# Optimization experiments

Hardware: AMD Instinct MI355X
Metric: run time of the kernel (lower is better)

## Reference

```python
import jax, jax.numpy as jnp
import numpy as np

Q = 256    # ques_size (feat_size)
H = 256    # seq_hidden_size
T = 500000 # history length
K = 32     # attn_k


def setup_inputs() -> dict:
    key = jax.random.key(0)
    ks = jax.random.split(key, 10)
    s = 0.05
    return {
        "ques_h": jax.random.normal(ks[0], (Q,), dtype=jnp.float32),
        "score": jax.random.uniform(ks[1], (1,), dtype=jnp.float32),
        "qs": jax.random.normal(ks[2], (T, Q), dtype=jnp.float32),
        "hs": jax.random.normal(ks[3], (T, H), dtype=jnp.float32),
        # GRU params (torch gate order: reset, update, new)
        "W_ih": jax.random.normal(ks[4], (3 * H, 2 * Q), dtype=jnp.float32) * s,
        "W_hh": jax.random.normal(ks[5], (3 * H, H), dtype=jnp.float32) * s,
        "b_ih": jax.random.normal(ks[6], (3 * H,), dtype=jnp.float32) * s,
        "b_hh": jax.random.normal(ks[7], (3 * H,), dtype=jnp.float32) * s,
        # score_net: Linear(Q + H, 1)
        "W_s": jax.random.normal(ks[8], (1, Q + H), dtype=jnp.float32) * s,
        "b_s": jax.random.normal(ks[9], (1,), dtype=jnp.float32) * s,
        "attn_k": K,
    }


def reference(ques_h, score, qs, hs, W_ih, W_hh, b_ih, b_hh, W_s, b_s, attn_k):
    # --- top-k attention over history ---
    alpha = qs @ ques_h                       # [T] similarity matvec
    vals, idx = jax.lax.top_k(alpha, attn_k)  # k = min(T, attn_k); T >> k
    w = jax.nn.softmax(vals)                  # [k]
    attn_h = w @ hs[idx]                      # gather [k,H] then weighted sum -> [H]

    # --- score prediction ---
    pred = W_s @ jnp.concatenate([ques_h, attn_h]) + b_s  # [1]

    # --- score-gated GRU input ---
    ge = (score >= 0.5).astype(ques_h.dtype)              # [1], broadcasts
    x = jnp.concatenate([ques_h * ge, ques_h * (1.0 - ge)])  # [2Q]

    # --- single-step GRU (torch semantics) ---
    h_prev = hs[-1]                            # [H]
    gi = W_ih @ x + b_ih                       # [3H]
    gh = W_hh @ h_prev + b_hh                  # [3H]
    i_r, i_z, i_n = jnp.split(gi, 3)
    h_r, h_z, h_n = jnp.split(gh, 3)
    r = jax.nn.sigmoid(i_r + h_r)
    z = jax.nn.sigmoid(i_z + h_z)
    n = jnp.tanh(i_n + r * h_n)
    h_new = (1.0 - z) * n + z * h_prev         # [H]

    # --- history append (torch.cat bookkeeping in SP.forward) ---
    qs_new = jnp.concatenate([qs, ques_h[None, :]], axis=0)  # [T+1, Q]
    hs_new = jnp.concatenate([hs, h_new[None, :]], axis=0)   # [T+1, H]
    return (pred, qs_new, hs_new)
```

## Files before the change

kernel.cpp:

```cpp
#include <hip/hip_runtime.h>
#include <math.h>

constexpr int kT = 500000;
constexpr int kQ = 256;
constexpr int kH = 256;
constexpr int kK = 32;
constexpr int kNB1 = 256;
constexpr int kCHUNK = (kT + kNB1 - 1) / kNB1;
constexpr int kNC = kNB1 * kK;

__device__ __forceinline__ void store4(float* __restrict__ dst, float4 v) {
  dst[0] = v.x; dst[1] = v.y; dst[2] = v.z; dst[3] = v.w;
}

__global__ __launch_bounds__(256) void k_copy_qs_alpha(
    const float* __restrict__ qs, const float* __restrict__ qh,
    float* __restrict__ out, float* __restrict__ alpha) {
  const int lane = threadIdx.x & 63;
  const int wid  = (int)((blockIdx.x * blockDim.x + threadIdx.x) >> 6);
  const int nw   = (int)((gridDim.x * blockDim.x) >> 6);
  const float4 q4 = ((const float4*)qh)[lane];
  for (int t = wid; t <= kT; t += nw) {
    const float4* src = (t < kT) ? ((const float4*)(qs + (size_t)t * kQ))
                                 : ((const float4*)qh);
    float4 v = src[lane];
    store4(out + 1 + (size_t)t * kQ + lane * 4, v);
    if (t < kT) {
      float d = v.x * q4.x + v.y * q4.y + v.z * q4.z + v.w * q4.w;
#pragma unroll
      for (int off = 32; off; off >>= 1) d += __shfl_xor(d, off);
      if (lane == 0) alpha[t] = d;
    }
  }
}

__global__ __launch_bounds__(256) void k_copy_hs(
    const float* __restrict__ hs, float* __restrict__ out) {
  const size_t i      = (size_t)blockIdx.x * blockDim.x + threadIdx.x;
  const size_t stride = (size_t)gridDim.x * blockDim.x;
  float* base = out + 1 + (size_t)(kT + 1) * kQ;
  const float4* src = (const float4*)hs;
  const size_t nv = (size_t)kT * (kH / 4);
  for (size_t v = i; v < nv; v += stride) {
    store4(base + v * 4, src[v]);
  }
}

__global__ __launch_bounds__(256) void k_topk1(
    const float* __restrict__ alpha, float* __restrict__ candV,
    int* __restrict__ candI) {
  __shared__ float sv[kCHUNK];
  __shared__ float rv[4];
  __shared__ int ri[4];
  const int tid = threadIdx.x;
  const int base = blockIdx.x * kCHUNK;
  for (int i = tid; i < kCHUNK; i += 256) {
    int g = base + i;
    sv[i] = (g < kT) ? alpha[g] : -INFINITY;
  }
  __syncthreads();
  for (int k = 0; k < kK; ++k) {
    float bv = -INFINITY; int bi = -1;
    for (int i = tid; i < kCHUNK; i += 256) {
      float v = sv[i];
      if (v > bv) { bv = v; bi = i; }
    }
#pragma unroll
    for (int off = 32; off; off >>= 1) {
      float ov = __shfl_xor(bv, off);
      int   oi = __shfl_xor(bi, off);
      if (ov > bv || (ov == bv && oi != -1 && (bi == -1 || oi < bi))) { bv = ov; bi = oi; }
    }
    if ((tid & 63) == 0) { rv[tid >> 6] = bv; ri[tid >> 6] = bi; }
    __syncthreads();
    if (tid == 0) {
      float fv = rv[0]; int fi = ri[0];
      for (int j = 1; j < 4; ++j)
        if (rv[j] > fv || (rv[j] == fv && ri[j] != -1 && (fi == -1 || ri[j] < fi))) {
          fv = rv[j]; fi = ri[j];
        }
      candV[blockIdx.x * kK + k] = fv;
      candI[blockIdx.x * kK + k] = (fi >= 0) ? (base + fi) : 0;
      if (fi >= 0) sv[fi] = -INFINITY;
    }
    __syncthreads();
  }
}

__global__ __launch_bounds__(256) void k_attn(
    const float* __restrict__ candV, const int* __restrict__ candI,
    const float* __restrict__ hs, const float* __restrict__ qh,
    const float* __restrict__ Ws, const float* __restrict__ bs,
    float* __restrict__ out) {
  __shared__ float sv[kNC];
  __shared__ float rv[4];
  __shared__ int ri[4];
  __shared__ float topv[kK];
  __shared__ int topi[kK];
  __shared__ float w[kK];
  __shared__ float red[256];
  const int tid = threadIdx.x;
  for (int i = tid; i < kNC; i += 256) sv[i] = candV[i];
  __syncthreads();
  for (int k = 0; k < kK; ++k) {
    float bv = -INFINITY; int bi = -1;
    for (int i = tid; i < kNC; i += 256) {
      float v = sv[i];
      if (v > bv) { bv = v; bi = i; }
    }
#pragma unroll
    for (int off = 32; off; off >>= 1) {
      float ov = __shfl_xor(bv, off);
      int   oi = __shfl_xor(bi, off);
      if (ov > bv || (ov == bv && oi != -1 && (bi == -1 || oi < bi))) { bv = ov; bi = oi; }
    }
    if ((tid & 63) == 0) { rv[tid >> 6] = bv; ri[tid >> 6] = bi; }
    __syncthreads();
    if (tid == 0) {
      float fv = rv[0]; int fi = ri[0];
      for (int j = 1; j < 4; ++j)
        if (rv[j] > fv || (rv[j] == fv && ri[j] != -1 && (fi == -1 || ri[j] < fi))) {
          fv = rv[j]; fi = ri[j];
        }
      topv[k] = fv;
      topi[k] = candI[fi];
      sv[fi] = -INFINITY;
    }
    __syncthreads();
  }
  if (tid == 0) {
    float m = topv[0];
    for (int j = 1; j < kK; ++j) m = fmaxf(m, topv[j]);
    float s = 0.f;
    for (int j = 0; j < kK; ++j) { w[j] = expf(topv[j] - m); s += w[j]; }
    float inv = 1.f / s;
    for (int j = 0; j < kK; ++j) w[j] *= inv;
  }
  __syncthreads();
  float a = 0.f;
#pragma unroll
  for (int j = 0; j < kK; ++j) a += w[j] * hs[(size_t)topi[j] * kH + tid];
  red[tid] = Ws[tid] * qh[tid] + Ws[kQ + tid] * a;
  __syncthreads();
  for (int s = 128; s; s >>= 1) {
    if (tid < s) red[tid] += red[tid + s];
    __syncthreads();
  }
  if (tid == 0) out[0] = red[0] + bs[0];
}

__global__ __launch_bounds__(64) void k_gru1(
    const float* __restrict__ Wih, const float* __restrict__ Whh,
    const float* __restrict__ bih, const float* __restrict__ bhh,
    const float* __restrict__ qh, const float* __restrict__ hs,
    const float* __restrict__ score, float* __restrict__ gi,
    float* __restrict__ gh) {
  const int r = blockIdx.x;
  const int lane = threadIdx.x;
  const int off = (score[0] >= 0.5f) ? 0 : kQ;
  const float* hprev = hs + (size_t)(kT - 1) * kH;
  float4 q4 = ((const float4*)qh)[lane];
  float4 h4 = ((const float4*)hprev)[lane];
  float4 wi = ((const float4*)(Wih + (size_t)r * (2 * kQ) + off))[lane];
  float4 wh = ((const float4*)(Whh + (size_t)r * kH))[lane];
  float di = wi.x * q4.x + wi.y * q4.y + wi.z * q4.z + wi.w * q4.w;
  float dh = wh.x * h4.x + wh.y * h4.y + wh.z * h4.z + wh.w * h4.w;
#pragma unroll
  for (int o = 32; o; o >>= 1) {
    di += __shfl_xor(di, o);
    dh += __shfl_xor(dh, o);
  }
  if (lane == 0) {
    gi[r] = di + bih[r];
    gh[r] = dh + bhh[r];
  }
}

__global__ __launch_bounds__(256) void k_gru2(
    const float* __restrict__ gi, const float* __restrict__ gh,
    const float* __restrict__ hs, float* __restrict__ out) {
  const int i = threadIdx.x;
  const float* hprev = hs + (size_t)(kT - 1) * kH;
  float rr = 1.f / (1.f + expf(-(gi[i] + gh[i])));
  float z  = 1.f / (1.f + expf(-(gi[kH + i] + gh[kH + i])));
  float n  = tanhf(gi[2 * kH + i] + rr * gh[2 * kH + i]);
  float hn = (1.f - z) * n + z * hprev[i];
  out[1 + (size_t)(kT + 1) * kQ + (size_t)kT * kH + i] = hn;
}

extern "C" void kernel_launch(void* const* d_in, const int* in_sizes, int n_in,
                              void* d_out, int out_size, void* d_ws, size_t ws_size,
                              hipStream_t stream) {
  const float* qh    = (const float*)d_in[0];
  const float* score = (const float*)d_in[1];
  const float* qs    = (const float*)d_in[2];
  const float* hs    = (const float*)d_in[3];
  const float* Wih   = (const float*)d_in[4];
  const float* Whh   = (const float*)d_in[5];
  const float* bih   = (const float*)d_in[6];
  const float* bhh   = (const float*)d_in[7];
  const float* Ws    = (const float*)d_in[8];
  const float* bs    = (const float*)d_in[9];
  float* out = (float*)d_out;

  float* S     = out + 1 + (size_t)(kT + 1) * kQ;
  float* alpha = S;
  float* candV = S + kT;
  int*   candI = (int*)(S + kT + kNC);
  float* gi    = S + kT + 2 * kNC;
  float* gh    = gi + 3 * kH;

  hipLaunchKernelGGL(k_copy_qs_alpha, dim3(2048), dim3(256), 0, stream,
                     qs, qh, out, alpha);
  hipLaunchKernelGGL(k_topk1, dim3(kNB1), dim3(256), 0, stream,
                     alpha, candV, candI);
  hipLaunchKernelGGL(k_attn, dim3(1), dim3(256), 0, stream,
                     candV, candI, hs, qh, Ws, bs, out);
  hipLaunchKernelGGL(k_gru1, dim3(3 * kH), dim3(64), 0, stream,
                     Wih, Whh, bih, bhh, qh, hs, score, gi, gh);
  hipLaunchKernelGGL(k_gru2, dim3(1), dim3(256), 0, stream,
                     gi, gh, hs, out);
  hipLaunchKernelGGL(k_copy_hs, dim3(2048), dim3(256), 0, stream,
                     hs, out);
}
```

Measured before the change: 586.4 us.

## Fuse hs copy into qs pass and merge GRU kernels with top-k stages

When a workspace buffer is large enough, scratch arrays move out of the output tensor, so the hs copy can run inside the same grid-stride kernel as the qs copy and the alpha matvec. The GRU gate matvec becomes extra blocks of the first-stage top-k kernel, and the GRU elementwise step becomes a second block of the attention kernel, which cuts six launches down to three. Stores now use a single 4-wide vector write at 4-byte alignment instead of four scalar stores. The fallback path keeps a separate hs copy when no workspace is available.

```diff
diff --git a/kernel.cpp b/kernel.cpp
--- a/kernel.cpp
+++ b/kernel.cpp
@@ -8,28 +8,39 @@
 constexpr int kNB1 = 256;
 constexpr int kCHUNK = (kT + kNB1 - 1) / kNB1;
 constexpr int kNC = kNB1 * kK;
-
-__device__ __forceinline__ void store4(float* __restrict__ dst, float4 v) {
-  dst[0] = v.x; dst[1] = v.y; dst[2] = v.z; dst[3] = v.w;
-}
-
-__global__ __launch_bounds__(256) void k_copy_qs_alpha(
-    const float* __restrict__ qs, const float* __restrict__ qh,
-    float* __restrict__ out, float* __restrict__ alpha) {
+constexpr int kGruRows = 3 * kH;
+constexpr int kGruBlocks = kGruRows / 4;
+
+typedef float f4  __attribute__((ext_vector_type(4)));
+typedef float f4u __attribute__((ext_vector_type(4), aligned(4)));
+
+constexpr size_t kScratchFloats = (size_t)kT + 2 * kNC + 2 * kGruRows;
+
+__global__ __launch_bounds__(256) void k_bigcopy(
+    const float* __restrict__ qs, const float* __restrict__ hs,
+    const float* __restrict__ qh, float* __restrict__ out,
+    float* __restrict__ alpha, int doHs) {
   const int lane = threadIdx.x & 63;
   const int wid  = (int)((blockIdx.x * blockDim.x + threadIdx.x) >> 6);
   const int nw   = (int)((gridDim.x * blockDim.x) >> 6);
-  const float4 q4 = ((const float4*)qh)[lane];
-  for (int t = wid; t <= kT; t += nw) {
-    const float4* src = (t < kT) ? ((const float4*)(qs + (size_t)t * kQ))
-                                 : ((const float4*)qh);
-    float4 v = src[lane];
-    store4(out + 1 + (size_t)t * kQ + lane * 4, v);
-    if (t < kT) {
-      float d = v.x * q4.x + v.y * q4.y + v.z * q4.z + v.w * q4.w;
-#pragma unroll
-      for (int off = 32; off; off >>= 1) d += __shfl_xor(d, off);
-      if (lane == 0) alpha[t] = d;
+  const f4 q4 = ((const f4*)qh)[lane];
+  const int totalRows = doHs ? (2 * kT + 1) : (kT + 1);
+  for (int t = wid; t < totalRows; t += nw) {
+    if (t <= kT) {
+      const f4* src = (t < kT) ? (const f4*)(qs + (size_t)t * kQ)
+                               : (const f4*)qh;
+      f4 v = src[lane];
+      *(f4u*)(out + 1 + (size_t)t * kQ + lane * 4) = v;
+      if (t < kT) {
+        float d = v.x * q4.x + v.y * q4.y + v.z * q4.z + v.w * q4.w;
+#pragma unroll
+        for (int off = 32; off; off >>= 1) d += __shfl_xor(d, off);
+        if (lane == 0) alpha[t] = d;
+      }
+    } else {
+      const int r = t - (kT + 1);
+      f4 v = ((const f4*)(hs + (size_t)r * kH))[lane];
+      *(f4u*)(out + 1 + (size_t)(kT + 1) * kQ + (size_t)r * kH + lane * 4) = v;
     }
   }
 }
@@ -39,20 +50,47 @@
   const size_t i      = (size_t)blockIdx.x * blockDim.x + threadIdx.x;
   const size_t stride = (size_t)gridDim.x * blockDim.x;
   float* base = out + 1 + (size_t)(kT + 1) * kQ;
-  const float4* src = (const float4*)hs;
+  const f4* src = (const f4*)hs;
   const size_t nv = (size_t)kT * (kH / 4);
   for (size_t v = i; v < nv; v += stride) {
-    store4(base + v * 4, src[v]);
-  }
-}
-
-__global__ __launch_bounds__(256) void k_topk1(
+    *(f4u*)(base + v * 4) = src[v];
+  }
+}
+
+__global__ __launch_bounds__(256) void k_topk_gru(
     const float* __restrict__ alpha, float* __restrict__ candV,
-    int* __restrict__ candI) {
+    int* __restrict__ candI,
+    const float* __restrict__ Wih, const float* __restrict__ Whh,
+    const float* __restrict__ bih, const float* __restrict__ bhh,
+    const float* __restrict__ qh, const float* __restrict__ hs,
+    const float* __restrict__ score, float* __restrict__ gi,
+    float* __restrict__ gh) {
+  const int tid = threadIdx.x;
+  if (blockIdx.x >= kNB1) {
+    const int lane = tid & 63;
+    const int r = (blockIdx.x - kNB1) * 4 + (tid >> 6);
+    const int off = (score[0] >= 0.5f) ? 0 : kQ;
+    const float* hprev = hs + (size_t)(kT - 1) * kH;
+    f4 q4 = ((const f4*)qh)[lane];
+    f4 h4 = ((const f4*)hprev)[lane];
+    f4 wi = ((const f4*)(Wih + (size_t)r * (2 * kQ) + off))[lane];
+    f4 wh = ((const f4*)(Whh + (size_t)r * kH))[lane];
+    float di = wi.x * q4.x + wi.y * q4.y + wi.z * q4.z + wi.w * q4.w;
+    float dh = wh.x * h4.x + wh.y * h4.y + wh.z * h4.z + wh.w * h4.w;
+#pragma unroll
+    for (int o = 32; o; o >>= 1) {
+      di += __shfl_xor(di, o);
+      dh += __shfl_xor(dh, o);
+    }
+    if (lane == 0) {
+      gi[r] = di + bih[r];
+      gh[r] = dh + bhh[r];
+    }
+    return;
+  }
   __shared__ float sv[kCHUNK];
   __shared__ float rv[4];
   __shared__ int ri[4];
-  const int tid = threadIdx.x;
   const int base = blockIdx.x * kCHUNK;
   for (int i = tid; i < kCHUNK; i += 256) {
     int g = base + i;
@@ -87,11 +125,22 @@
   }
 }
 
-__global__ __launch_bounds__(256) void k_attn(
+__global__ __launch_bounds__(256) void k_attn_gru2(
     const float* __restrict__ candV, const int* __restrict__ candI,
     const float* __restrict__ hs, const float* __restrict__ qh,
     const float* __restrict__ Ws, const float* __restrict__ bs,
+    const float* __restrict__ gi, const float* __restrict__ gh,
     float* __restrict__ out) {
+  const int tid = threadIdx.x;
+  if (blockIdx.x == 1) {
+    const float* hprev = hs + (size_t)(kT - 1) * kH;
+    float rr = 1.f / (1.f + expf(-(gi[tid] + gh[tid])));
+    float z  = 1.f / (1.f + expf(-(gi[kH + tid] + gh[kH + tid])));
+    float n  = tanhf(gi[2 * kH + tid] + rr * gh[2 * kH + tid]);
+    float hn = (1.f - z) * n + z * hprev[tid];
+    out[1 + (size_t)(kT + 1) * kQ + (size_t)kT * kH + tid] = hn;
+    return;
+  }
   __shared__ float sv[kNC];
   __shared__ float rv[4];
   __shared__ int ri[4];
@@ -99,7 +148,6 @@
   __shared__ int topi[kK];
   __shared__ float w[kK];
   __shared__ float red[256];
-  const int tid = threadIdx.x;
   for (int i = tid; i < kNC; i += 256) sv[i] = candV[i];
   __syncthreads();
   for (int k = 0; k < kK; ++k) {
@@ -147,45 +195,6 @@
     __syncthreads();
   }
   if (tid == 0) out[0] = red[0] + bs[0];
-}
-
-__global__ __launch_bounds__(64) void k_gru1(
-    const float* __restrict__ Wih, const float* __restrict__ Whh,
-    const float* __restrict__ bih, const float* __restrict__ bhh,
-    const float* __restrict__ qh, const float* __restrict__ hs,
-    const float* __restrict__ score, float* __restrict__ gi,
-    float* __restrict__ gh) {
-  const int r = blockIdx.x;
-  const int lane = threadIdx.x;
-  const int off = (score[0] >= 0.5f) ? 0 : kQ;
-  const float* hprev = hs + (size_t)(kT - 1) * kH;
-  float4 q4 = ((const float4*)qh)[lane];
-  float4 h4 = ((const float4*)hprev)[lane];
-  float4 wi = ((const float4*)(Wih + (size_t)r * (2 * kQ) + off))[lane];
-  float4 wh = ((const float4*)(Whh + (size_t)r * kH))[lane];
-  float di = wi.x * q4.x + wi.y * q4.y + wi.z * q4.z + wi.w * q4.w;
-  float dh = wh.x * h4.x + wh.y * h4.y + wh.z * h4.z + wh.w * h4.w;
-#pragma unroll
-  for (int o = 32; o; o >>= 1) {
-    di += __shfl_xor(di, o);
-    dh += __shfl_xor(dh, o);
-  }
-  if (lane == 0) {
-    gi[r] = di + bih[r];
-    gh[r] = dh + bhh[r];
-  }
-}
-
-__global__ __launch_bounds__(256) void k_gru2(
-    const float* __restrict__ gi, const float* __restrict__ gh,
-    const float* __restrict__ hs, float* __restrict__ out) {
-  const int i = threadIdx.x;
-  const float* hprev = hs + (size_t)(kT - 1) * kH;
-  float rr = 1.f / (1.f + expf(-(gi[i] + gh[i])));
-  float z  = 1.f / (1.f + expf(-(gi[kH + i] + gh[kH + i])));
-  float n  = tanhf(gi[2 * kH + i] + rr * gh[2 * kH + i]);
-  float hn = (1.f - z) * n + z * hprev[i];
-  out[1 + (size_t)(kT + 1) * kQ + (size_t)kT * kH + i] = hn;
 }
 
 extern "C" void kernel_launch(void* const* d_in, const int* in_sizes, int n_in,
@@ -203,23 +212,31 @@
   const float* bs    = (const float*)d_in[9];
   float* out = (float*)d_out;
 
-  float* S     = out + 1 + (size_t)(kT + 1) * kQ;
+  const bool useWs = ws_size >= kScratchFloats * sizeof(float);
+  float* S = useWs ? (float*)d_ws : (out + 1 + (size_t)(kT + 1) * kQ);
   float* alpha = S;
   float* candV = S + kT;
   int*   candI = (int*)(S + kT + kNC);
   float* gi    = S + kT + 2 * kNC;
-  float* gh    = gi + 3 * kH;
-
-  hipLaunchKernelGGL(k_copy_qs_alpha, dim3(2048), dim3(256), 0, stream,
-                     qs, qh, out, alpha);
-  hipLaunchKernelGGL(k_topk1, dim3(kNB1), dim3(256), 0, stream,
-                     alpha, candV, candI);
-  hipLaunchKernelGGL(k_attn, dim3(1), dim3(256), 0, stream,
-                     candV, candI, hs, qh, Ws, bs, out);
-  hipLaunchKernelGGL(k_gru1, dim3(3 * kH), dim3(64), 0, stream,
-                     Wih, Whh, bih, bhh, qh, hs, score, gi, gh);
-  hipLaunchKernelGGL(k_gru2, dim3(1), dim3(256), 0, stream,
-                     gi, gh, hs, out);
-  hipLaunchKernelGGL(k_copy_hs, dim3(2048), dim3(256), 0, stream,
-                     hs, out);
-}
+  float* gh    = gi + kGruRows;
+
+  if (useWs) {
+    hipLaunchKernelGGL(k_bigcopy, dim3(2048), dim3(256), 0, stream,
+                       qs, hs, qh, out, alpha, 1);
+    hipLaunchKernelGGL(k_topk_gru, dim3(kNB1 + kGruBlocks), dim3(256), 0, stream,
+                       alpha, candV, candI, Wih, Whh, bih, bhh, qh, hs, score,
+                       gi, gh);
+    hipLaunchKernelGGL(k_attn_gru2, dim3(2), dim3(256), 0, stream,
+                       candV, candI, hs, qh, Ws, bs, gi, gh, out);
+  } else {
+    hipLaunchKernelGGL(k_bigcopy, dim3(2048), dim3(256), 0, stream,
+                       qs, hs, qh, out, alpha, 0);
+    hipLaunchKernelGGL(k_topk_gru, dim3(kNB1 + kGruBlocks), dim3(256), 0, stream,
+                       alpha, candV, candI, Wih, Whh, bih, bhh, qh, hs, score,
+                       gi, gh);
+    hipLaunchKernelGGL(k_attn_gru2, dim3(2), dim3(256), 0, stream,
+                       candV, candI, hs, qh, Ws, bs, gi, gh, out);
+    hipLaunchKernelGGL(k_copy_hs, dim3(2048), dim3(256), 0, stream,
+                       hs, out);
+  }
+}
```

Result: no change. 593.2 us (+1.2%).

## Merge qs/hs copies into one kernel with aligned vector stores and workspace scratch

Applied to the files above, without the earlier changes.

Combines the qs copy plus alpha matvec and the hs copy into a single grid-stride kernel over all output rows. Stores are realigned through a lane shuffle so each lane writes an aligned 16-byte vector, replacing four scalar stores at the odd offset left by the leading pred element. The GRU runs first, and its new hidden state is staged in a workspace scratch buffer so the final hs row can be written by the same copy kernel. The GRU matvec now packs four rows per block, which adds shuffles and branching per row in return for wider stores and fewer launches.

```diff
diff --git a/kernel.cpp b/kernel.cpp
--- a/kernel.cpp
+++ b/kernel.cpp
@@ -8,42 +8,85 @@
 constexpr int kNB1 = 256;
 constexpr int kCHUNK = (kT + kNB1 - 1) / kNB1;
 constexpr int kNC = kNB1 * kK;
-
-__device__ __forceinline__ void store4(float* __restrict__ dst, float4 v) {
-  dst[0] = v.x; dst[1] = v.y; dst[2] = v.z; dst[3] = v.w;
-}
-
-__global__ __launch_bounds__(256) void k_copy_qs_alpha(
-    const float* __restrict__ qs, const float* __restrict__ qh,
-    float* __restrict__ out, float* __restrict__ alpha) {
+constexpr int kGruRows = 3 * kH;
+constexpr int kGruBlocks = kGruRows / 4;
+constexpr int kRowsQs = kT + 1;
+constexpr int kRowsAll = 2 * kT + 2;
+
+typedef float f4 __attribute__((ext_vector_type(4)));
+
+constexpr size_t kScratchFloats = (size_t)kT + 2 * kNC + 2 * kGruRows + kH;
+
+__global__ __launch_bounds__(256) void k_bigcopy(
+    const float* __restrict__ qs, const float* __restrict__ hs,
+    const float* __restrict__ qh, const float* __restrict__ hnew,
+    float* __restrict__ out, float* __restrict__ alpha,
+    int rowBegin, int rowEnd) {
   const int lane = threadIdx.x & 63;
   const int wid  = (int)((blockIdx.x * blockDim.x + threadIdx.x) >> 6);
   const int nw   = (int)((gridDim.x * blockDim.x) >> 6);
-  const float4 q4 = ((const float4*)qh)[lane];
-  for (int t = wid; t <= kT; t += nw) {
-    const float4* src = (t < kT) ? ((const float4*)(qs + (size_t)t * kQ))
-                                 : ((const float4*)qh);
-    float4 v = src[lane];
-    store4(out + 1 + (size_t)t * kQ + lane * 4, v);
-    if (t < kT) {
+  const f4 q4 = ((const f4*)qh)[lane];
+  for (int r = rowBegin + wid; r < rowEnd; r += nw) {
+    const f4* src;
+    if (r < kT)               src = (const f4*)(qs + (size_t)r * kQ);
+    else if (r == kT)         src = (const f4*)qh;
+    else if (r < 2 * kT + 1)  src = (const f4*)(hs + (size_t)(r - kT - 1) * kH);
+    else                      src = (const f4*)hnew;
+    f4 v = src[lane];
+    float pw = __shfl_up(v.w, 1);
+    float* obase = out + 1 + (size_t)r * kQ;
+    if (lane > 0) {
+      f4 sv; sv.x = pw; sv.y = v.x; sv.z = v.y; sv.w = v.z;
+      *(f4*)(obase - 1 + 4 * lane) = sv;
+    } else {
+      obase[0] = v.x; obase[1] = v.y; obase[2] = v.z;
+    }
+    if (lane == 63) obase[255] = v.w;
+    if (r < kT) {
       float d = v.x * q4.x + v.y * q4.y + v.z * q4.z + v.w * q4.w;
 #pragma unroll
       for (int off = 32; off; off >>= 1) d += __shfl_xor(d, off);
-      if (lane == 0) alpha[t] = d;
-    }
-  }
-}
-
-__global__ __launch_bounds__(256) void k_copy_hs(
-    const float* __restrict__ hs, float* __restrict__ out) {
-  const size_t i      = (size_t)blockIdx.x * blockDim.x + threadIdx.x;
-  const size_t stride = (size_t)gridDim.x * blockDim.x;
-  float* base = out + 1 + (size_t)(kT + 1) * kQ;
-  const float4* src = (const float4*)hs;
-  const size_t nv = (size_t)kT * (kH / 4);
-  for (size_t v = i; v < nv; v += stride) {
-    store4(base + v * 4, src[v]);
-  }
+      if (lane == 0) alpha[r] = d;
+    }
+  }
+}
+
+__global__ __launch_bounds__(256) void k_gru1(
+    const float* __restrict__ Wih, const float* __restrict__ Whh,
+    const float* __restrict__ bih, const float* __restrict__ bhh,
+    const float* __restrict__ qh, const float* __restrict__ hs,
+    const float* __restrict__ score, float* __restrict__ gi,
+    float* __restrict__ gh) {
+  const int lane = threadIdx.x & 63;
+  const int r = blockIdx.x * 4 + (threadIdx.x >> 6);
+  const int off = (score[0] >= 0.5f) ? 0 : kQ;
+  const float* hprev = hs + (size_t)(kT - 1) * kH;
+  f4 q4 = ((const f4*)qh)[lane];
+  f4 h4 = ((const f4*)hprev)[lane];
+  f4 wi = ((const f4*)(Wih + (size_t)r * (2 * kQ) + off))[lane];
+  f4 wh = ((const f4*)(Whh + (size_t)r * kH))[lane];
+  float di = wi.x * q4.x + wi.y * q4.y + wi.z * q4.z + wi.w * q4.w;
+  float dh = wh.x * h4.x + wh.y * h4.y + wh.z * h4.z + wh.w * h4.w;
+#pragma unroll
+  for (int o = 32; o; o >>= 1) {
+    di += __shfl_xor(di, o);
+    dh += __shfl_xor(dh, o);
+  }
+  if (lane == 0) {
+    gi[r] = di + bih[r];
+    gh[r] = dh + bhh[r];
+  }
+}
+
+__global__ __launch_bounds__(256) void k_gru2(
+    const float* __restrict__ gi, const float* __restrict__ gh,
+    const float* __restrict__ hs, float* __restrict__ hnew_dst) {
+  const int i = threadIdx.x;
+  const float* hprev = hs + (size_t)(kT - 1) * kH;
+  float rr = 1.f / (1.f + expf(-(gi[i] + gh[i])));
+  float z  = 1.f / (1.f + expf(-(gi[kH + i] + gh[kH + i])));
+  float n  = tanhf(gi[2 * kH + i] + rr * gh[2 * kH + i]);
+  hnew_dst[i] = (1.f - z) * n + z * hprev[i];
 }
 
 __global__ __launch_bounds__(256) void k_topk1(
@@ -149,45 +192,6 @@
   if (tid == 0) out[0] = red[0] + bs[0];
 }
 
-__global__ __launch_bounds__(64) void k_gru1(
-    const float* __restrict__ Wih, const float* __restrict__ Whh,
-    const float* __restrict__ bih, const float* __restrict__ bhh,
-    const float* __restrict__ qh, const float* __restrict__ hs,
-    const float* __restrict__ score, float* __restrict__ gi,
-    float* __restrict__ gh) {
-  const int r = blockIdx.x;
-  const int lane = threadIdx.x;
-  const int off = (score[0] >= 0.5f) ? 0 : kQ;
-  const float* hprev = hs + (size_t)(kT - 1) * kH;
-  float4 q4 = ((const float4*)qh)[lane];
-  float4 h4 = ((const float4*)hprev)[lane];
-  float4 wi = ((const float4*)(Wih + (size_t)r * (2 * kQ) + off))[lane];
-  float4 wh = ((const float4*)(Whh + (size_t)r * kH))[lane];
-  float di = wi.x * q4.x + wi.y * q4.y + wi.z * q4.z + wi.w * q4.w;
-  float dh = wh.x * h4.x + wh.y * h4.y + wh.z * h4.z + wh.w * h4.w;
-#pragma unroll
-  for (int o = 32; o; o >>= 1) {
-    di += __shfl_xor(di, o);
-    dh += __shfl_xor(dh, o);
-  }
-  if (lane == 0) {
-    gi[r] = di + bih[r];
-    gh[r] = dh + bhh[r];
-  }
-}
-
-__global__ __launch_bounds__(256) void k_gru2(
-    const float* __restrict__ gi, const float* __restrict__ gh,
-    const float* __restrict__ hs, float* __restrict__ out) {
-  const int i = threadIdx.x;
-  const float* hprev = hs + (size_t)(kT - 1) * kH;
-  float rr = 1.f / (1.f + expf(-(gi[i] + gh[i])));
-  float z  = 1.f / (1.f + expf(-(gi[kH + i] + gh[kH + i])));
-  float n  = tanhf(gi[2 * kH + i] + rr * gh[2 * kH + i]);
-  float hn = (1.f - z) * n + z * hprev[i];
-  out[1 + (size_t)(kT + 1) * kQ + (size_t)kT * kH + i] = hn;
-}
-
 extern "C" void kernel_launch(void* const* d_in, const int* in_sizes, int n_in,
                               void* d_out, int out_size, void* d_ws, size_t ws_size,
                               hipStream_t stream) {
@@ -203,23 +207,39 @@
   const float* bs    = (const float*)d_in[9];
   float* out = (float*)d_out;
 
-  float* S     = out + 1 + (size_t)(kT + 1) * kQ;
+  const bool useWs = ws_size >= kScratchFloats * sizeof(float);
+  float* S = useWs ? (float*)d_ws : (out + 1 + (size_t)(kT + 1) * kQ);
   float* alpha = S;
   float* candV = S + kT;
   int*   candI = (int*)(S + kT + kNC);
   float* gi    = S + kT + 2 * kNC;
-  float* gh    = gi + 3 * kH;
-
-  hipLaunchKernelGGL(k_copy_qs_alpha, dim3(2048), dim3(256), 0, stream,
-                     qs, qh, out, alpha);
-  hipLaunchKernelGGL(k_topk1, dim3(kNB1), dim3(256), 0, stream,
-                     alpha, candV, candI);
-  hipLaunchKernelGGL(k_attn, dim3(1), dim3(256), 0, stream,
-                     candV, candI, hs, qh, Ws, bs, out);
-  hipLaunchKernelGGL(k_gru1, dim3(3 * kH), dim3(64), 0, stream,
-                     Wih, Whh, bih, bhh, qh, hs, score, gi, gh);
-  hipLaunchKernelGGL(k_gru2, dim3(1), dim3(256), 0, stream,
-                     gi, gh, hs, out);
-  hipLaunchKernelGGL(k_copy_hs, dim3(2048), dim3(256), 0, stream,
-                     hs, out);
-}
+  float* gh    = gi + kGruRows;
+  float* hnew  = gh + kGruRows;
+
+  if (useWs) {
+    hipLaunchKernelGGL(k_gru1, dim3(kGruBlocks), dim3(256), 0, stream,
+                       Wih, Whh, bih, bhh, qh, hs, score, gi, gh);
+    hipLaunchKernelGGL(k_gru2, dim3(1), dim3(256), 0, stream,
+                       gi, gh, hs, hnew);
+    hipLaunchKernelGGL(k_bigcopy, dim3(2048), dim3(256), 0, stream,
+                       qs, hs, qh, hnew, out, alpha, 0, kRowsAll);
+    hipLaunchKernelGGL(k_topk1, dim3(kNB1), dim3(256), 0, stream,
+                       alpha, candV, candI);
+    hipLaunchKernelGGL(k_attn, dim3(1), dim3(256), 0, stream,
+                       candV, candI, hs, qh, Ws, bs, out);
+  } else {
+    float* hnewOut = out + 1 + (size_t)(kT + 1) * kQ + (size_t)kT * kH;
+    hipLaunchKernelGGL(k_gru1, dim3(kGruBlocks), dim3(256), 0, stream,
+                       Wih, Whh, bih, bhh, qh, hs, score, gi, gh);
+    hipLaunchKernelGGL(k_gru2, dim3(1), dim3(256), 0, stream,
+                       gi, gh, hs, hnewOut);
+    hipLaunchKernelGGL(k_bigcopy, dim3(2048), dim3(256), 0, stream,
+                       qs, hs, qh, hnewOut, out, alpha, 0, kRowsQs);
+    hipLaunchKernelGGL(k_topk1, dim3(kNB1), dim3(256), 0, stream,
+                       alpha, candV, candI);
+    hipLaunchKernelGGL(k_attn, dim3(1), dim3(256), 0, stream,
+                       candV, candI, hs, qh, Ws, bs, out);
+    hipLaunchKernelGGL(k_bigcopy, dim3(2048), dim3(256), 0, stream,
+                       qs, hs, qh, hnewOut, out, alpha, kRowsQs, 2 * kT + 1);
+  }
+}
```

Result: slower. 604.1 us (+3.0%).
